# Performance work log

Hardware: AMD Instinct MI355X
Metric: run time of the kernel (lower is better)

The kernel has to match this reference:

```python
import jax, jax.numpy as jnp
import numpy as np

B, T, N, F, H, K = 16, 24, 1329, 130, 15, 5


def setup_inputs() -> dict:
    key = jax.random.key(0)
    ks = jax.random.split(key, 14)
    var1 = 2.0 / (N + F)
    var2 = 2.0 / (F + 1)
    return {
        "seq": jax.random.uniform(ks[0], (B, T, N), jnp.float32),
        "A_hat": jax.random.uniform(ks[1], (N, N), jnp.float32) / N,  # normalized-adjacency scale
        "weight": jax.random.normal(ks[2], (N, F), jnp.float32) * var1,
        "bias": jax.random.normal(ks[3], (F,), jnp.float32) * var1,
        "weight2": jax.random.normal(ks[4], (F, 1), jnp.float32) * var2,
        "bias2": jax.random.normal(ks[5], (1,), jnp.float32) * var2,
        "W_ih": jax.random.normal(ks[6], (4 * H, N), jnp.float32) * 0.05,
        "W_hh": jax.random.normal(ks[7], (4 * H, H), jnp.float32) * 0.05,
        "b_ih": jax.random.normal(ks[8], (4 * H,), jnp.float32) * 0.05,
        "b_hh": jax.random.normal(ks[9], (4 * H,), jnp.float32) * 0.05,
        "h0": jax.random.normal(ks[10], (B, H), jnp.float32),
        "c0": jax.random.normal(ks[11], (B, H), jnp.float32),
        "fc_w": jax.random.normal(ks[12], (K, N, H), jnp.float32) * 0.05,
        "fc_b": jax.random.normal(ks[13], (K, N), jnp.float32) * 0.05,
    }


def reference(seq, A_hat, weight, bias, weight2, bias2,
              W_ih, W_hh, b_ih, b_hh, h0, c0, fc_w, fc_b):
    # --- GCN part (vectorized over all batch/timestep pairs) ---
    # diag(seq[b,t]) @ weight == row-scale of weight by seq values
    X = seq[..., None] * weight + bias                       # [B,T,N,F]
    X = jax.nn.relu(jnp.einsum('mn,btnf->btmf', A_hat, X))   # [B,T,N,F]
    Y = jnp.einsum('btnf,fo->btno', X, weight2)[..., 0] + bias2  # [B,T,N]
    Y = jax.nn.relu(jnp.einsum('mn,btn->btm', A_hat, Y))     # [B,T,N]

    # --- LSTM (PyTorch gate order i, f, g, o) ---
    def step(carry, x_t):
        h, c = carry
        g = x_t @ W_ih.T + h @ W_hh.T + b_ih + b_hh          # [B,4H]
        i, f, gg, o = jnp.split(g, 4, axis=-1)
        c = jax.nn.sigmoid(f) * c + jax.nn.sigmoid(i) * jnp.tanh(gg)
        h = jax.nn.sigmoid(o) * jnp.tanh(c)
        return (h, c), None

    (h_last, _), _ = jax.lax.scan(step, (h0, c0), jnp.swapaxes(Y, 0, 1))

    # --- 5 FC heads on sigmoid(last hidden) ---
    s = jax.nn.sigmoid(h_last)                               # [B,H]
    outs = jnp.tanh(jnp.einsum('koh,bh->kbo', fc_w, s) + fc_b[:, None, :])  # [K,B,N]
    return tuple(outs[k] for k in range(K))
```

## Files before the change

kernel.cpp:

```cpp
#include <hip/hip_runtime.h>
#include <hip/hip_bf16.h>
#include <math.h>

#define NN 1329
#define FF 130
#define BB 16
#define TT 24
#define HH 15
#define KK 5
#define BT (BB*TT)
#define G4 (4*HH)

#define KPAD 1344
#define NKC 42
#define MFRAG 88
#define NMT 11
#define NCF 9
#define NBTF 24
#define NKCO 44

typedef __attribute__((ext_vector_type(8))) short short8v;
typedef __attribute__((ext_vector_type(4))) float f32x4;

#define OFS_ROWSUM 0
#define OFS_SPAD   1408
#define OFS_Y1     (OFS_SPAD + BT*KPAD)
#define OFS_XW     (OFS_Y1 + BT*NN)
#define OFS_S      (OFS_XW + BT*64)
#define OFS_END_F  (OFS_S + 256)
#define ABF_ELEMS  (NKC*MFRAG*64*8)
#define WBF_ELEMS  (NKC*NCF*64*8)
#define WTB_ELEMS  (NKC*4*64*8)
#define Y2A_ELEMS  (NKCO*NBTF*64*8)

__device__ __forceinline__ float sigmoidf(float x) { return 1.f / (1.f + expf(-x)); }

__device__ __forceinline__ unsigned short bf16rne(float x) {
    unsigned u = __float_as_uint(x);
    return (unsigned short)((u + 0x7fffu + ((u >> 16) & 1u)) >> 16);
}
__device__ __forceinline__ float bf16lo(unsigned a) { return __uint_as_float(a << 16); }
__device__ __forceinline__ float bf16hi(unsigned a) { return __uint_as_float(a & 0xffff0000u); }
__device__ __forceinline__ unsigned cvtpk2(float lo, float hi) {
    unsigned r;
    asm volatile("v_cvt_pk_bf16_f32 %0, %1, %2" : "=v"(r) : "v"(lo), "v"(hi));
    return r;
}

__device__ __forceinline__ void gll16(const void* g, void* l) {
    __builtin_amdgcn_global_load_lds((const __attribute__((address_space(1))) unsigned*)g,
                                     (__attribute__((address_space(3))) unsigned*)l, 16, 0, 0);
}

#define NB_APREP 924
#define NB_WPREP 95
#define NB_SPREP 2016
#define NB_WTB   42
#define NB_ROWS  NN
#define NB_PREP  (NB_APREP+NB_WPREP+NB_SPREP+NB_WTB+NB_ROWS)

__global__ __launch_bounds__(256) void k_prep(
    const float* __restrict__ A, const float* __restrict__ W,
    const float* __restrict__ seq, const float* __restrict__ Wih,
    unsigned short* __restrict__ Abf, unsigned short* __restrict__ Wbf,
    float* __restrict__ spad, unsigned short* __restrict__ WihTbf, float* __restrict__ rowsum)
{
    __shared__ float r4[4];
    const int bid = blockIdx.x;
    const int tid = threadIdx.x;
    if (bid < NB_APREP) {
        int s = bid*256 + tid;
        int l = s & 63;
        int t = s >> 6;
        int mf = t % MFRAG;
        int kcg = t / MFRAG;
        int m = mf*16 + (l & 15);
        int kb = kcg*32 + (l >> 4)*8;
        union { uint4 u4; unsigned short us[8]; } ow;
#pragma unroll
        for (int j = 0; j < 8; j++) {
            int k = kb + j;
            float x = (m < NN && k < NN) ? A[(size_t)m*NN + k] : 0.f;
            ow.us[j] = bf16rne(x);
        }
        *(uint4*)(Abf + (size_t)s*8) = ow.u4;
    } else if (bid < NB_APREP+NB_WPREP) {
        int s = (bid-NB_APREP)*256 + tid;
        if (s < NKC*NCF*64) {
            int l = s & 63;
            int t = s >> 6;
            int cf = t % NCF;
            int kcg = t / NCF;
            int f = cf*16 + (l & 15);
            int kb = kcg*32 + (l >> 4)*8;
            union { uint4 u4; unsigned short us[8]; } ow;
#pragma unroll
            for (int j = 0; j < 8; j++) {
                int k = kb + j;
                float x = (k < NN && f < FF) ? W[(size_t)k*FF + f] : 0.f;
                ow.us[j] = bf16rne(x);
            }
            *(uint4*)(Wbf + (size_t)s*8) = ow.u4;
        }
    } else if (bid < NB_APREP+NB_WPREP+NB_SPREP) {
        int idx = (bid-NB_APREP-NB_WPREP)*256 + tid;
        int bt = idx / KPAD;
        int k  = idx - bt*KPAD;
        spad[idx] = (k < NN) ? seq[(size_t)bt*NN + k] : 0.f;
    } else if (bid < NB_APREP+NB_WPREP+NB_SPREP+NB_WTB) {
        int s = (bid-NB_APREP-NB_WPREP-NB_SPREP)*256 + tid;
        int l = s & 63;
        int t = s >> 6;
        int gf = t & 3;
        int kcg = t >> 2;
        int g = gf*16 + (l & 15);
        int nb = kcg*32 + (l >> 4)*8;
        union { uint4 u4; unsigned short us[8]; } ow;
#pragma unroll
        for (int j = 0; j < 8; j++) {
            int n = nb + j;
            float x = (g < G4 && n < NN) ? Wih[(size_t)g*NN + n] : 0.f;
            ow.us[j] = bf16rne(x);
        }
        *(uint4*)(WihTbf + (size_t)s*8) = ow.u4;
    } else {
        int m = bid - (NB_APREP+NB_WPREP+NB_SPREP+NB_WTB);
        float a = 0.f;
        for (int n = tid; n < NN; n += 256) a += A[(size_t)m*NN + n];
#pragma unroll
        for (int off = 32; off; off >>= 1) a += __shfl_down(a, off, 64);
        if ((tid & 63) == 0) r4[tid >> 6] = a;
        __syncthreads();
        if (tid == 0) rowsum[m] = r4[0]+r4[1]+r4[2]+r4[3];
    }
}

__global__ __launch_bounds__(256,2) void k_gcn1(
    const unsigned short* __restrict__ Abf, const unsigned short* __restrict__ Wbf,
    const float* __restrict__ spad,
    const float* __restrict__ bias, const float* __restrict__ w2, const float* __restrict__ bias2,
    const float* __restrict__ rowsum, float* __restrict__ Y1)
{
    __shared__ __align__(16) short Blds[2][NCF*64*8];

    const int id = blockIdx.x;
    const int mt = id / BT;
    const int bt = id - mt*BT;
    const int m0 = mt*128;
    const int tid = threadIdx.x;
    const int lane = tid & 63;
    const int wv = tid >> 6;
    const float* sb = spad + (size_t)bt*KPAD;
    const int klane = (lane >> 4)*8;

    f32x4 acc[2][NCF];
#pragma unroll
    for (int rf = 0; rf < 2; rf++)
#pragma unroll
        for (int cf = 0; cf < NCF; cf++) acc[rf][cf] = (f32x4){0.f, 0.f, 0.f, 0.f};

    auto stageB = [&](int kcg, int nb) {
        const unsigned short* wsrc = Wbf + (size_t)kcg*(NCF*64*8);
#pragma unroll
        for (int it = 0; it < 2; ++it) {
            int slot = it*256 + tid;
            gll16(wsrc + (size_t)slot*8, &Blds[nb][slot*8]);
        }
        if (tid < 64) {
            int slot = 512 + tid;
            gll16(wsrc + (size_t)slot*8, &Blds[nb][slot*8]);
        }
    };
    uint4 r0, r1; float4 s0, s1;
    auto loadA = [&](int kcg) {
        const unsigned short* p = Abf + ((size_t)(kcg*MFRAG + mt*8 + 2*wv)*64 + lane)*8;
        r0 = *(const uint4*)p;
        r1 = *(const uint4*)(p + 64*8);
        const float* sp = sb + kcg*32 + klane;
        s0 = *(const float4*)sp;
        s1 = *(const float4*)(sp + 4);
    };
    auto scaleA = [&](uint4 r) -> short8v {
        union { uint4 u4; short8v s8; } o;
        o.u4.x = cvtpk2(bf16lo(r.x)*s0.x, bf16hi(r.x)*s0.y);
        o.u4.y = cvtpk2(bf16lo(r.y)*s0.z, bf16hi(r.y)*s0.w);
        o.u4.z = cvtpk2(bf16lo(r.z)*s1.x, bf16hi(r.z)*s1.y);
        o.u4.w = cvtpk2(bf16lo(r.w)*s1.z, bf16hi(r.w)*s1.w);
        return o.s8;
    };

    stageB(0, 0);
    loadA(0);
    __syncthreads();
    short8v a0 = scaleA(r0), a1 = scaleA(r1);

    for (int t = 0; t < NKC; ++t) {
        const int cur = t & 1;
        if (t + 1 < NKC) { stageB(t+1, cur^1); loadA(t+1); }
        short8v bfr[NCF];
#pragma unroll
        for (int cf = 0; cf < NCF; cf++)
            bfr[cf] = *(const short8v*)&Blds[cur][(cf*64 + lane)*8];
#pragma unroll
        for (int cf = 0; cf < NCF; cf++) {
            acc[0][cf] = __builtin_amdgcn_mfma_f32_16x16x32_bf16(a0, bfr[cf], acc[0][cf], 0, 0, 0);
            acc[1][cf] = __builtin_amdgcn_mfma_f32_16x16x32_bf16(a1, bfr[cf], acc[1][cf], 0, 0, 0);
        }
        if (t + 1 < NKC) { a0 = scaleA(r0); a1 = scaleA(r1); }
        __syncthreads();
    }

    const int fcol = lane & 15;
    const int rgrp = lane >> 4;
    float bv[NCF], wv2[NCF];
#pragma unroll
    for (int cf = 0; cf < NCF; cf++) {
        int f = cf*16 + fcol;
        bv[cf]  = (f < FF) ? bias[f] : 0.f;
        wv2[cf] = (f < FF) ? w2[f]   : 0.f;
    }
    float b2 = bias2[0];
#pragma unroll
    for (int rf = 0; rf < 2; rf++) {
#pragma unroll
        for (int r = 0; r < 4; r++) {
            int m = m0 + (2*wv + rf)*16 + rgrp*4 + r;
            float rs = (m < NN) ? rowsum[m] : 0.f;
            float p = 0.f;
#pragma unroll
            for (int cf = 0; cf < NCF; cf++)
                p += fmaxf(acc[rf][cf][r] + bv[cf]*rs, 0.f) * wv2[cf];
            p += __shfl_xor(p, 1, 64);
            p += __shfl_xor(p, 2, 64);
            p += __shfl_xor(p, 4, 64);
            p += __shfl_xor(p, 8, 64);
            if (fcol == 0 && m < NN) Y1[(size_t)bt*NN + m] = p + b2;
        }
    }
}

__global__ __launch_bounds__(256) void k_gcn2(
    const unsigned short* __restrict__ Abf, const float* __restrict__ Y1,
    unsigned short* __restrict__ Y2A)
{
    const int mt  = blockIdx.x;
    const int btg = blockIdx.y;
    const int tid = threadIdx.x;
    const int lane = tid & 63;
    const int wv = tid >> 6;
    const int q = lane >> 4;

    f32x4 acc[2][2];
#pragma unroll
    for (int rf = 0; rf < 2; rf++)
#pragma unroll
        for (int cf = 0; cf < 2; cf++) acc[rf][cf] = (f32x4){0.f, 0.f, 0.f, 0.f};

    const float* y1r0 = Y1 + (size_t)((btg*2 + 0)*16 + (lane & 15))*NN;
    const float* y1r1 = Y1 + (size_t)((btg*2 + 1)*16 + (lane & 15))*NN;
    const int nq = q*8;

    for (int kcg = 0; kcg < NKC; ++kcg) {
        const unsigned short* ap = Abf + ((size_t)(kcg*MFRAG + mt*8 + 2*wv)*64 + lane)*8;
        short8v a0 = *(const short8v*)ap;
        short8v a1 = *(const short8v*)(ap + 64*8);
        int n0 = kcg*32 + nq;
        union { uint4 u4; short8v s8; } b0, b1;
        if (kcg < NKC-1) {
            float4 x0 = *(const float4*)(y1r0 + n0);
            float4 x1 = *(const float4*)(y1r0 + n0 + 4);
            b0.u4.x = cvtpk2(x0.x, x0.y); b0.u4.y = cvtpk2(x0.z, x0.w);
            b0.u4.z = cvtpk2(x1.x, x1.y); b0.u4.w = cvtpk2(x1.z, x1.w);
            float4 y0 = *(const float4*)(y1r1 + n0);
            float4 y1v = *(const float4*)(y1r1 + n0 + 4);
            b1.u4.x = cvtpk2(y0.x, y0.y); b1.u4.y = cvtpk2(y0.z, y0.w);
            b1.u4.z = cvtpk2(y1v.x, y1v.y); b1.u4.w = cvtpk2(y1v.z, y1v.w);
        } else {
            float xa[8], xb[8];
#pragma unroll
            for (int j = 0; j < 8; j++) {
                int n = n0 + j;
                xa[j] = (n < NN) ? y1r0[n] : 0.f;
                xb[j] = (n < NN) ? y1r1[n] : 0.f;
            }
            b0.u4.x = cvtpk2(xa[0], xa[1]); b0.u4.y = cvtpk2(xa[2], xa[3]);
            b0.u4.z = cvtpk2(xa[4], xa[5]); b0.u4.w = cvtpk2(xa[6], xa[7]);
            b1.u4.x = cvtpk2(xb[0], xb[1]); b1.u4.y = cvtpk2(xb[2], xb[3]);
            b1.u4.z = cvtpk2(xb[4], xb[5]); b1.u4.w = cvtpk2(xb[6], xb[7]);
        }
        acc[0][0] = __builtin_amdgcn_mfma_f32_16x16x32_bf16(a0, b0.s8, acc[0][0], 0, 0, 0);
        acc[1][0] = __builtin_amdgcn_mfma_f32_16x16x32_bf16(a1, b0.s8, acc[1][0], 0, 0, 0);
        acc[0][1] = __builtin_amdgcn_mfma_f32_16x16x32_bf16(a0, b1.s8, acc[0][1], 0, 0, 0);
        acc[1][1] = __builtin_amdgcn_mfma_f32_16x16x32_bf16(a1, b1.s8, acc[1][1], 0, 0, 0);
    }

    const int kcgo = mt*4 + wv;
    const int jofs = (q & 1)*4;
#pragma unroll
    for (int rf = 0; rf < 2; rf++) {
        int lp = (rf*2 + (q >> 1))*16 + (lane & 15);
#pragma unroll
        for (int cf = 0; cf < 2; cf++) {
            int btf = btg*2 + cf;
            uint2 w2v;
            w2v.x = cvtpk2(fmaxf(acc[rf][cf][0], 0.f), fmaxf(acc[rf][cf][1], 0.f));
            w2v.y = cvtpk2(fmaxf(acc[rf][cf][2], 0.f), fmaxf(acc[rf][cf][3], 0.f));
            *(uint2*)(Y2A + ((size_t)(kcgo*NBTF + btf)*64 + lp)*8 + jofs) = w2v;
        }
    }
}

__global__ __launch_bounds__(64) void k_xwm(
    const unsigned short* __restrict__ Y2A, const unsigned short* __restrict__ WihTbf,
    float* __restrict__ xW)
{
    const int btf = blockIdx.x;
    const int lane = threadIdx.x;
    f32x4 acc[4];
#pragma unroll
    for (int gf = 0; gf < 4; gf++) acc[gf] = (f32x4){0.f, 0.f, 0.f, 0.f};

    for (int kcg = 0; kcg < NKC; ++kcg) {
        short8v a = *(const short8v*)(Y2A + ((size_t)(kcg*NBTF + btf)*64 + lane)*8);
#pragma unroll
        for (int gf = 0; gf < 4; gf++) {
            short8v b = *(const short8v*)(WihTbf + ((size_t)(kcg*4 + gf)*64 + lane)*8);
            acc[gf] = __builtin_amdgcn_mfma_f32_16x16x32_bf16(a, b, acc[gf], 0, 0, 0);
        }
    }
#pragma unroll
    for (int gf = 0; gf < 4; gf++)
#pragma unroll
        for (int r = 0; r < 4; r++) {
            int bt = btf*16 + (lane >> 4)*4 + r;
            xW[(size_t)bt*64 + gf*16 + (lane & 15)] = acc[gf][r];
        }
}

__global__ __launch_bounds__(64) void k_lstm(const float* __restrict__ xW,
    const float* __restrict__ Whh, const float* __restrict__ bih, const float* __restrict__ bhh,
    const float* __restrict__ h0, const float* __restrict__ c0, float* __restrict__ s_out)
{
    __shared__ float h_s[16];
    int b = blockIdx.x;
    int lane = threadIdx.x;
    float whh_r[HH];
    float bs = 0.f;
    if (lane < G4) {
        bs = bih[lane] + bhh[lane];
#pragma unroll
        for (int k = 0; k < HH; k++) whh_r[k] = Whh[lane*HH + k];
    }
    float c_r = 0.f, h_last = 0.f;
    if (lane < HH) { h_s[lane] = h0[b*HH + lane]; c_r = c0[b*HH + lane]; }
    __syncthreads();
    for (int t = 0; t < TT; ++t) {
        float v = 0.f;
        if (lane < G4) {
            v = xW[(size_t)(b*TT + t)*64 + lane] + bs;
#pragma unroll
            for (int k = 0; k < HH; k++) v = fmaf(whh_r[k], h_s[k], v);
        }
        float vi = __shfl(v, lane, 64);
        float vf = __shfl(v, HH   + lane, 64);
        float vg = __shfl(v, 2*HH + lane, 64);
        float vo = __shfl(v, 3*HH + lane, 64);
        __syncthreads();
        if (lane < HH) {
            float c = sigmoidf(vf)*c_r + sigmoidf(vi)*tanhf(vg);
            c_r = c;
            float h = sigmoidf(vo)*tanhf(c);
            h_s[lane] = h;
            h_last = h;
        }
        __syncthreads();
    }
    if (lane < HH) s_out[b*HH + lane] = sigmoidf(h_last);
}

__global__ __launch_bounds__(256) void k_heads(const float* __restrict__ fc_w,
    const float* __restrict__ fc_b, const float* __restrict__ s, float* __restrict__ out)
{
    __shared__ float s_s[BB*HH];
    int tid = threadIdx.x;
    if (tid < BB*HH) s_s[tid] = s[tid];
    __syncthreads();
    int idx = blockIdx.x*256 + tid;
    if (idx >= KK*BB*NN) return;
    int k = idx / (BB*NN);
    int rem = idx - k*(BB*NN);
    int b = rem / NN;
    int n = rem - b*NN;
    const float* wp = fc_w + ((size_t)k*NN + n)*HH;
    const float* sp = s_s + b*HH;
    float v = fc_b[k*NN + n];
#pragma unroll
    for (int h = 0; h < HH; h++) v = fmaf(wp[h], sp[h], v);
    out[idx] = tanhf(v);
}

extern "C" void kernel_launch(void* const* d_in, const int* in_sizes, int n_in,
                              void* d_out, int out_size, void* d_ws, size_t ws_size,
                              hipStream_t stream) {
    const float* seq   = (const float*)d_in[0];
    const float* A     = (const float*)d_in[1];
    const float* W     = (const float*)d_in[2];
    const float* bias  = (const float*)d_in[3];
    const float* w2    = (const float*)d_in[4];
    const float* bias2 = (const float*)d_in[5];
    const float* Wih   = (const float*)d_in[6];
    const float* Whh   = (const float*)d_in[7];
    const float* bih   = (const float*)d_in[8];
    const float* bhh   = (const float*)d_in[9];
    const float* h0    = (const float*)d_in[10];
    const float* c0    = (const float*)d_in[11];
    const float* fcw   = (const float*)d_in[12];
    const float* fcb   = (const float*)d_in[13];
    float* ws = (float*)d_ws;
    float* rowsum = ws + OFS_ROWSUM;
    float* spad   = ws + OFS_SPAD;
    float* Y1     = ws + OFS_Y1;
    float* xW     = ws + OFS_XW;
    float* s_sig  = ws + OFS_S;
    unsigned short* Abf    = (unsigned short*)(ws + OFS_END_F);
    unsigned short* Wbf    = Abf + ABF_ELEMS;
    unsigned short* WihTbf = Wbf + WBF_ELEMS;
    unsigned short* Y2A    = WihTbf + WTB_ELEMS;
    float* out = (float*)d_out;

    hipLaunchKernelGGL(k_prep, dim3(NB_PREP), dim3(256), 0, stream,
                       A, W, seq, Wih, Abf, Wbf, spad, WihTbf, rowsum);
    hipLaunchKernelGGL(k_gcn1, dim3(NMT*BT), dim3(256), 0, stream,
                       Abf, Wbf, spad, bias, w2, bias2, rowsum, Y1);
    hipLaunchKernelGGL(k_gcn2, dim3(NMT, 12), dim3(256), 0, stream, Abf, Y1, Y2A);
    hipLaunchKernelGGL(k_xwm, dim3(NBTF), dim3(64), 0, stream, Y2A, WihTbf, xW);
    hipLaunchKernelGGL(k_lstm, dim3(BB), dim3(64), 0, stream, xW, Whh, bih, bhh, h0, c0, s_sig);
    hipLaunchKernelGGL(k_heads, dim3((KK*BB*NN + 255)/256), dim3(256), 0, stream, fcw, fcb, s_sig, out);
}
```

Measured before the change: 367.6 us.

## Reuse A fragments across two bt slices in gcn1 and fuse LSTM tail kernels

k_gcn1 now handles two batch-time slices per block, so each bf16 A fragment load and each staged weight tile feeds twice as many MFMAs, and the grid is halved. The xW matmul, the LSTM recurrence and the FC heads are merged into one per-batch kernel that keeps xW and the sigmoid state in LDS, which removes two launches and their global round trips. The costs are a doubled accumulator footprint in gcn1, which raises register pressure and may reduce occupancy, and a tail whose FC heads now run on only 16 blocks, recomputing over fc_w once per batch.

New measurement: 369.3 us. About the same (+0.5%).

```diff
diff --git a/kernel.cpp b/kernel.cpp
--- a/kernel.cpp
+++ b/kernel.cpp
@@ -18,6 +18,7 @@
 #define NCF 9
 #define NBTF 24
 #define NKCO 44
+#define NBTP 192
 
 typedef __attribute__((ext_vector_type(8))) short short8v;
 typedef __attribute__((ext_vector_type(4))) float f32x4;
@@ -25,9 +26,7 @@
 #define OFS_ROWSUM 0
 #define OFS_SPAD   1408
 #define OFS_Y1     (OFS_SPAD + BT*KPAD)
-#define OFS_XW     (OFS_Y1 + BT*NN)
-#define OFS_S      (OFS_XW + BT*64)
-#define OFS_END_F  (OFS_S + 256)
+#define OFS_END_F  (OFS_Y1 + BT*NN)
 #define ABF_ELEMS  (NKC*MFRAG*64*8)
 #define WBF_ELEMS  (NKC*NCF*64*8)
 #define WTB_ELEMS  (NKC*4*64*8)
@@ -144,20 +143,25 @@
     __shared__ __align__(16) short Blds[2][NCF*64*8];
 
     const int id = blockIdx.x;
-    const int mt = id / BT;
-    const int bt = id - mt*BT;
+    const int mt = id / NBTP;
+    const int btp = id - mt*NBTP;
+    const int bt0 = btp, bt1 = btp + NBTP;
     const int m0 = mt*128;
     const int tid = threadIdx.x;
     const int lane = tid & 63;
     const int wv = tid >> 6;
-    const float* sb = spad + (size_t)bt*KPAD;
+    const float* sba = spad + (size_t)bt0*KPAD;
+    const float* sbb = spad + (size_t)bt1*KPAD;
     const int klane = (lane >> 4)*8;
 
-    f32x4 acc[2][NCF];
+    f32x4 accA[2][NCF], accB[2][NCF];
 #pragma unroll
     for (int rf = 0; rf < 2; rf++)
 #pragma unroll
-        for (int cf = 0; cf < NCF; cf++) acc[rf][cf] = (f32x4){0.f, 0.f, 0.f, 0.f};
+        for (int cf = 0; cf < NCF; cf++) {
+            accA[rf][cf] = (f32x4){0.f, 0.f, 0.f, 0.f};
+            accB[rf][cf] = (f32x4){0.f, 0.f, 0.f, 0.f};
+        }
 
     auto stageB = [&](int kcg, int nb) {
         const unsigned short* wsrc = Wbf + (size_t)kcg*(NCF*64*8);
@@ -171,16 +175,20 @@
             gll16(wsrc + (size_t)slot*8, &Blds[nb][slot*8]);
         }
     };
-    uint4 r0, r1; float4 s0, s1;
+    uint4 r0, r1;
+    float4 s0a, s1a, s0b, s1b;
     auto loadA = [&](int kcg) {
         const unsigned short* p = Abf + ((size_t)(kcg*MFRAG + mt*8 + 2*wv)*64 + lane)*8;
         r0 = *(const uint4*)p;
         r1 = *(const uint4*)(p + 64*8);
-        const float* sp = sb + kcg*32 + klane;
-        s0 = *(const float4*)sp;
-        s1 = *(const float4*)(sp + 4);
+        const float* spa = sba + kcg*32 + klane;
+        s0a = *(const float4*)spa;
+        s1a = *(const float4*)(spa + 4);
+        const float* spb = sbb + kcg*32 + klane;
+        s0b = *(const float4*)spb;
+        s1b = *(const float4*)(spb + 4);
     };
-    auto scaleA = [&](uint4 r) -> short8v {
+    auto scaleA = [&](uint4 r, float4 s0, float4 s1) -> short8v {
         union { uint4 u4; short8v s8; } o;
         o.u4.x = cvtpk2(bf16lo(r.x)*s0.x, bf16hi(r.x)*s0.y);
         o.u4.y = cvtpk2(bf16lo(r.y)*s0.z, bf16hi(r.y)*s0.w);
@@ -192,21 +200,24 @@
     stageB(0, 0);
     loadA(0);
     __syncthreads();
-    short8v a0 = scaleA(r0), a1 = scaleA(r1);
+    short8v a0a = scaleA(r0, s0a, s1a), a1a = scaleA(r1, s0a, s1a);
+    short8v a0b = scaleA(r0, s0b, s1b), a1b = scaleA(r1, s0b, s1b);
 
     for (int t = 0; t < NKC; ++t) {
         const int cur = t & 1;
         if (t + 1 < NKC) { stageB(t+1, cur^1); loadA(t+1); }
-        short8v bfr[NCF];
-#pragma unroll
-        for (int cf = 0; cf < NCF; cf++)
-            bfr[cf] = *(const short8v*)&Blds[cur][(cf*64 + lane)*8];
 #pragma unroll
         for (int cf = 0; cf < NCF; cf++) {
-            acc[0][cf] = __builtin_amdgcn_mfma_f32_16x16x32_bf16(a0, bfr[cf], acc[0][cf], 0, 0, 0);
-            acc[1][cf] = __builtin_amdgcn_mfma_f32_16x16x32_bf16(a1, bfr[cf], acc[1][cf], 0, 0, 0);
-        }
-        if (t + 1 < NKC) { a0 = scaleA(r0); a1 = scaleA(r1); }
+            short8v bfr = *(const short8v*)&Blds[cur][(cf*64 + lane)*8];
+            accA[0][cf] = __builtin_amdgcn_mfma_f32_16x16x32_bf16(a0a, bfr, accA[0][cf], 0, 0, 0);
+            accA[1][cf] = __builtin_amdgcn_mfma_f32_16x16x32_bf16(a1a, bfr, accA[1][cf], 0, 0, 0);
+            accB[0][cf] = __builtin_amdgcn_mfma_f32_16x16x32_bf16(a0b, bfr, accB[0][cf], 0, 0, 0);
+            accB[1][cf] = __builtin_amdgcn_mfma_f32_16x16x32_bf16(a1b, bfr, accB[1][cf], 0, 0, 0);
+        }
+        if (t + 1 < NKC) {
+            a0a = scaleA(r0, s0a, s1a); a1a = scaleA(r1, s0a, s1a);
+            a0b = scaleA(r0, s0b, s1b); a1b = scaleA(r1, s0b, s1b);
+        }
         __syncthreads();
     }
 
@@ -221,20 +232,26 @@
     }
     float b2 = bias2[0];
 #pragma unroll
-    for (int rf = 0; rf < 2; rf++) {
-#pragma unroll
-        for (int r = 0; r < 4; r++) {
-            int m = m0 + (2*wv + rf)*16 + rgrp*4 + r;
-            float rs = (m < NN) ? rowsum[m] : 0.f;
-            float p = 0.f;
-#pragma unroll
-            for (int cf = 0; cf < NCF; cf++)
-                p += fmaxf(acc[rf][cf][r] + bv[cf]*rs, 0.f) * wv2[cf];
-            p += __shfl_xor(p, 1, 64);
-            p += __shfl_xor(p, 2, 64);
-            p += __shfl_xor(p, 4, 64);
-            p += __shfl_xor(p, 8, 64);
-            if (fcol == 0 && m < NN) Y1[(size_t)bt*NN + m] = p + b2;
+    for (int half = 0; half < 2; half++) {
+        int btv = half ? bt1 : bt0;
+#pragma unroll
+        for (int rf = 0; rf < 2; rf++) {
+#pragma unroll
+            for (int r = 0; r < 4; r++) {
+                int m = m0 + (2*wv + rf)*16 + rgrp*4 + r;
+                float rs = (m < NN) ? rowsum[m] : 0.f;
+                float p = 0.f;
+#pragma unroll
+                for (int cf = 0; cf < NCF; cf++) {
+                    float x = (half ? accB[rf][cf][r] : accA[rf][cf][r]) + bv[cf]*rs;
+                    p += fmaxf(x, 0.f) * wv2[cf];
+                }
+                p += __shfl_xor(p, 1, 64);
+                p += __shfl_xor(p, 2, 64);
+                p += __shfl_xor(p, 4, 64);
+                p += __shfl_xor(p, 8, 64);
+                if (fcol == 0 && m < NN) Y1[(size_t)btv*NN + m] = p + b2;
+            }
         }
     }
 }
@@ -310,93 +327,86 @@
     }
 }
 
-__global__ __launch_bounds__(64) void k_xwm(
+__global__ __launch_bounds__(256) void k_tail(
     const unsigned short* __restrict__ Y2A, const unsigned short* __restrict__ WihTbf,
-    float* __restrict__ xW)
+    const float* __restrict__ Whh, const float* __restrict__ bih, const float* __restrict__ bhh,
+    const float* __restrict__ h0, const float* __restrict__ c0,
+    const float* __restrict__ fc_w, const float* __restrict__ fc_b, float* __restrict__ out)
 {
-    const int btf = blockIdx.x;
-    const int lane = threadIdx.x;
-    f32x4 acc[4];
-#pragma unroll
-    for (int gf = 0; gf < 4; gf++) acc[gf] = (f32x4){0.f, 0.f, 0.f, 0.f};
-
-    for (int kcg = 0; kcg < NKC; ++kcg) {
-        short8v a = *(const short8v*)(Y2A + ((size_t)(kcg*NBTF + btf)*64 + lane)*8);
-#pragma unroll
-        for (int gf = 0; gf < 4; gf++) {
-            short8v b = *(const short8v*)(WihTbf + ((size_t)(kcg*4 + gf)*64 + lane)*8);
-            acc[gf] = __builtin_amdgcn_mfma_f32_16x16x32_bf16(a, b, acc[gf], 0, 0, 0);
-        }
-    }
-#pragma unroll
-    for (int gf = 0; gf < 4; gf++)
-#pragma unroll
-        for (int r = 0; r < 4; r++) {
-            int bt = btf*16 + (lane >> 4)*4 + r;
-            xW[(size_t)bt*64 + gf*16 + (lane & 15)] = acc[gf][r];
-        }
-}
-
-__global__ __launch_bounds__(64) void k_lstm(const float* __restrict__ xW,
-    const float* __restrict__ Whh, const float* __restrict__ bih, const float* __restrict__ bhh,
-    const float* __restrict__ h0, const float* __restrict__ c0, float* __restrict__ s_out)
-{
+    __shared__ float xw_lds[2][16][64];
     __shared__ float h_s[16];
-    int b = blockIdx.x;
-    int lane = threadIdx.x;
-    float whh_r[HH];
-    float bs = 0.f;
-    if (lane < G4) {
-        bs = bih[lane] + bhh[lane];
-#pragma unroll
-        for (int k = 0; k < HH; k++) whh_r[k] = Whh[lane*HH + k];
-    }
-    float c_r = 0.f, h_last = 0.f;
-    if (lane < HH) { h_s[lane] = h0[b*HH + lane]; c_r = c0[b*HH + lane]; }
+    __shared__ float s_sh[16];
+
+    const int b = blockIdx.x;
+    const int tid = threadIdx.x;
+    const int lane = tid & 63;
+    const int wv = tid >> 6;
+    const int f0 = (24*b) >> 4;
+
+    if (wv < 2) {
+        const int fw = f0 + wv;
+        f32x4 a4[4];
+#pragma unroll
+        for (int gf = 0; gf < 4; gf++) a4[gf] = (f32x4){0.f, 0.f, 0.f, 0.f};
+        for (int kcg = 0; kcg < NKC; ++kcg) {
+            short8v a = *(const short8v*)(Y2A + ((size_t)(kcg*NBTF + fw)*64 + lane)*8);
+#pragma unroll
+            for (int gf = 0; gf < 4; gf++) {
+                short8v bm = *(const short8v*)(WihTbf + ((size_t)(kcg*4 + gf)*64 + lane)*8);
+                a4[gf] = __builtin_amdgcn_mfma_f32_16x16x32_bf16(a, bm, a4[gf], 0, 0, 0);
+            }
+        }
+#pragma unroll
+        for (int gf = 0; gf < 4; gf++)
+#pragma unroll
+            for (int r = 0; r < 4; r++)
+                xw_lds[wv][(lane >> 4)*4 + r][gf*16 + (lane & 15)] = a4[gf][r];
+    }
     __syncthreads();
-    for (int t = 0; t < TT; ++t) {
-        float v = 0.f;
+
+    if (wv == 0) {
+        float whh_r[HH];
+        float bs = 0.f;
         if (lane < G4) {
-            v = xW[(size_t)(b*TT + t)*64 + lane] + bs;
-#pragma unroll
-            for (int k = 0; k < HH; k++) v = fmaf(whh_r[k], h_s[k], v);
-        }
-        float vi = __shfl(v, lane, 64);
-        float vf = __shfl(v, HH   + lane, 64);
-        float vg = __shfl(v, 2*HH + lane, 64);
-        float vo = __shfl(v, 3*HH + lane, 64);
-        __syncthreads();
-        if (lane < HH) {
-            float c = sigmoidf(vf)*c_r + sigmoidf(vi)*tanhf(vg);
-            c_r = c;
-            float h = sigmoidf(vo)*tanhf(c);
-            h_s[lane] = h;
-            h_last = h;
-        }
-        __syncthreads();
-    }
-    if (lane < HH) s_out[b*HH + lane] = sigmoidf(h_last);
-}
-
-__global__ __launch_bounds__(256) void k_heads(const float* __restrict__ fc_w,
-    const float* __restrict__ fc_b, const float* __restrict__ s, float* __restrict__ out)
-{
-    __shared__ float s_s[BB*HH];
-    int tid = threadIdx.x;
-    if (tid < BB*HH) s_s[tid] = s[tid];
+            bs = bih[lane] + bhh[lane];
+#pragma unroll
+            for (int k = 0; k < HH; k++) whh_r[k] = Whh[lane*HH + k];
+        }
+        float c_r = 0.f, h_last = 0.f;
+        if (lane < HH) { h_s[lane] = h0[b*HH + lane]; c_r = c0[b*HH + lane]; }
+        for (int t = 0; t < TT; ++t) {
+            int fidx = 24*b + t - f0*16;
+            float v = 0.f;
+            if (lane < G4) {
+                v = xw_lds[fidx >> 4][fidx & 15][lane] + bs;
+#pragma unroll
+                for (int k = 0; k < HH; k++) v = fmaf(whh_r[k], h_s[k], v);
+            }
+            float vi = __shfl(v, lane, 64);
+            float vf = __shfl(v, HH   + lane, 64);
+            float vg = __shfl(v, 2*HH + lane, 64);
+            float vo = __shfl(v, 3*HH + lane, 64);
+            if (lane < HH) {
+                float c = sigmoidf(vf)*c_r + sigmoidf(vi)*tanhf(vg);
+                c_r = c;
+                float h = sigmoidf(vo)*tanhf(c);
+                h_s[lane] = h;
+                h_last = h;
+            }
+        }
+        if (lane < HH) s_sh[lane] = sigmoidf(h_last);
+    }
     __syncthreads();
-    int idx = blockIdx.x*256 + tid;
-    if (idx >= KK*BB*NN) return;
-    int k = idx / (BB*NN);
-    int rem = idx - k*(BB*NN);
-    int b = rem / NN;
-    int n = rem - b*NN;
-    const float* wp = fc_w + ((size_t)k*NN + n)*HH;
-    const float* sp = s_s + b*HH;
-    float v = fc_b[k*NN + n];
-#pragma unroll
-    for (int h = 0; h < HH; h++) v = fmaf(wp[h], sp[h], v);
-    out[idx] = tanhf(v);
+
+    for (int idx = tid; idx < KK*NN; idx += 256) {
+        int k = idx / NN;
+        int n = idx - k*NN;
+        const float* wp = fc_w + (size_t)idx*HH;
+        float v = fc_b[idx];
+#pragma unroll
+        for (int h = 0; h < HH; h++) v = fmaf(wp[h], s_sh[h], v);
+        out[((size_t)k*BB + b)*NN + n] = tanhf(v);
+    }
 }
 
 extern "C" void kernel_launch(void* const* d_in, const int* in_sizes, int n_in,
@@ -420,8 +430,6 @@
     float* rowsum = ws + OFS_ROWSUM;
     float* spad   = ws + OFS_SPAD;
     float* Y1     = ws + OFS_Y1;
-    float* xW     = ws + OFS_XW;
-    float* s_sig  = ws + OFS_S;
     unsigned short* Abf    = (unsigned short*)(ws + OFS_END_F);
     unsigned short* Wbf    = Abf + ABF_ELEMS;
     unsigned short* WihTbf = Wbf + WBF_ELEMS;
@@ -430,10 +438,9 @@
 
     hipLaunchKernelGGL(k_prep, dim3(NB_PREP), dim3(256), 0, stream,
                        A, W, seq, Wih, Abf, Wbf, spad, WihTbf, rowsum);
-    hipLaunchKernelGGL(k_gcn1, dim3(NMT*BT), dim3(256), 0, stream,
+    hipLaunchKernelGGL(k_gcn1, dim3(NMT*NBTP), dim3(256), 0, stream,
                        Abf, Wbf, spad, bias, w2, bias2, rowsum, Y1);
     hipLaunchKernelGGL(k_gcn2, dim3(NMT, 12), dim3(256), 0, stream, Abf, Y1, Y2A);
-    hipLaunchKernelGGL(k_xwm, dim3(NBTF), dim3(64), 0, stream, Y2A, WihTbf, xW);
-    hipLaunchKernelGGL(k_lstm, dim3(BB), dim3(64), 0, stream, xW, Whh, bih, bhh, h0, c0, s_sig);
-    hipLaunchKernelGGL(k_heads, dim3((KK*BB*NN + 255)/256), dim3(256), 0, stream, fcw, fcb, s_sig, out);
-}
+    hipLaunchKernelGGL(k_tail, dim3(BB), dim3(256), 0, stream,
+                       Y2A, WihTbf, Whh, bih, bhh, h0, c0, fcw, fcb, out);
+}
```
